# Kernel tuning notes

Hardware: AMD Instinct MI355X
Metric: run time of the kernel (lower is better)

The kernel has to match this reference:

```python
import jax, jax.numpy as jnp
import numpy as np

RATIO = 0.5
TEMP = 0.1


def setup_inputs() -> dict:
    key = jax.random.key(0)
    k1, k2, k3 = jax.random.split(key, 3)
    B, D = 4096, 4096
    im = jax.random.normal(k1, (B, D), dtype=jnp.float32)
    s = jax.random.normal(k2, (2 * B, D), dtype=jnp.float32)
    sims_local = jax.random.normal(k3, (B, 2 * B), dtype=jnp.float32)
    return {"im": im, "s": s, "sims_local": sims_local}


def reference(im, s, sims_local):
    B = im.shape[0]
    # fused global + local similarity: [B, 2B]
    sim = RATIO * sims_local + (1.0 - RATIO) * (im @ s.T)
    diag = jnp.diagonal(sim[:, :B])  # positives, [B]
    # vectorized replacement of the python double loop: zero out second-half
    # columns that exceed the row's diagonal (diagonal lives in first half,
    # so updates never feed back into the comparison -> exact equivalence).
    second = jnp.where(sim[:, B:] > diag[:, None], 0.0, sim[:, B:])
    sim = jnp.concatenate([sim[:, :B], second], axis=1)

    # i2t: logits per row = [positive (diag), all other 2B-1 entries];
    # CE with label 0 == logsumexp(full row) - positive (permutation-invariant).
    logits_i2t = sim / TEMP
    loss_i2t = jnp.mean(jax.nn.logsumexp(logits_i2t, axis=1) - diag / TEMP)

    # t2i: transpose, keep first B rows -> first block transposed, [B, B]
    t = sim[:, :B].T
    logits_t2i = t / TEMP
    loss_t2i = jnp.mean(jax.nn.logsumexp(logits_t2i, axis=1) - jnp.diagonal(t) / TEMP)

    return loss_i2t + loss_t2i
```

## Files before the change

### kernel.cpp

```cpp
#include <hip/hip_runtime.h>
#include <hip/hip_bf16.h>

typedef __attribute__((ext_vector_type(8))) short short8;
typedef __attribute__((ext_vector_type(4))) float floatx4;

#define B_ROWS 4096
#define N_COLS 8192
#define K_DIM  4096
#define INV_T  10.0f

__device__ __forceinline__ unsigned pack2bf16(float a, float b) {
    unsigned lo = (__float_as_uint(a) + 0x8000u) >> 16;
    unsigned hi = (__float_as_uint(b) + 0x8000u) & 0xFFFF0000u;
    return lo | hi;
}

__device__ __forceinline__ void gload_lds16(const void* g, void* l) {
    __builtin_amdgcn_global_load_lds(
        (const __attribute__((address_space(1))) void*)g,
        (__attribute__((address_space(3))) void*)l,
        16, 0, 0);
}

__global__ __launch_bounds__(256) void convert_diag_kernel(
    const float* __restrict__ im, const float* __restrict__ s,
    const float* __restrict__ sims,
    unsigned short* __restrict__ im_b, unsigned short* __restrict__ s_b,
    float* __restrict__ diag)
{
    const int row = blockIdx.x;
    const float4* srow = (const float4*)(s + (size_t)row * K_DIM);
    uint4* sb = (uint4*)(s_b + (size_t)row * K_DIM);
    const bool has_im = row < B_ROWS;
    const float4* arow = (const float4*)(im + (size_t)row * K_DIM);
    uint4* ab = (uint4*)(im_b + (size_t)row * K_DIM);

    float sum = 0.f;
    for (int i = threadIdx.x; i < K_DIM / 8; i += 256) {
        float4 y0 = srow[2 * i], y1 = srow[2 * i + 1];
        sb[i] = make_uint4(pack2bf16(y0.x, y0.y), pack2bf16(y0.z, y0.w),
                           pack2bf16(y1.x, y1.y), pack2bf16(y1.z, y1.w));
        if (has_im) {
            float4 x0 = arow[2 * i], x1 = arow[2 * i + 1];
            ab[i] = make_uint4(pack2bf16(x0.x, x0.y), pack2bf16(x0.z, x0.w),
                               pack2bf16(x1.x, x1.y), pack2bf16(x1.z, x1.w));
            sum += x0.x * y0.x + x0.y * y0.y + x0.z * y0.z + x0.w * y0.w;
            sum += x1.x * y1.x + x1.y * y1.y + x1.z * y1.z + x1.w * y1.w;
        }
    }
    if (has_im) {
        #pragma unroll
        for (int off = 1; off < 64; off <<= 1) sum += __shfl_xor(sum, off, 64);
        __shared__ float wsum[4];
        const int lane = threadIdx.x & 63, wid = threadIdx.x >> 6;
        if (lane == 0) wsum[wid] = sum;
        __syncthreads();
        if (threadIdx.x == 0) {
            float tot = wsum[0] + wsum[1] + wsum[2] + wsum[3];
            diag[row] = 0.5f * sims[(size_t)row * N_COLS + row] + 0.5f * tot;
        }
    }
}

__global__ __launch_bounds__(256, 3) void gemm_loss_bf16_kernel(
    const unsigned short* __restrict__ im_b, const unsigned short* __restrict__ s_b,
    const float* __restrict__ sims, const float* __restrict__ diag,
    float* __restrict__ pi2t_m, float* __restrict__ pi2t_l,
    float* __restrict__ pt2i_m, float* __restrict__ pt2i_l)
{
    const int jt = blockIdx.x;
    const int it = blockIdx.y;
    const int tid = threadIdx.x;
    const int wid = tid >> 6, lane = tid & 63;
    const int wr = wid >> 1, wc = wid & 1;
    const int q = lane >> 4, cl = lane & 15;

    __shared__ __align__(16) unsigned short Asm[2][128 * 32];
    __shared__ __align__(16) unsigned short Bsm[2][128 * 32];
    __shared__ float sm_m[2][128], sm_l[2][128];
    __shared__ float sc_m[2][128], sc_l[2][128];

    const int r0 = (wid * 2 + 0) * 16 + (lane >> 2);
    const int r1 = (wid * 2 + 1) * 16 + (lane >> 2);
    const int kg = (((lane & 3) ^ ((lane >> 3) & 3))) * 8;
    const unsigned short* gA0 = im_b + (size_t)(it * 128 + r0) * K_DIM + kg;
    const unsigned short* gA1 = im_b + (size_t)(it * 128 + r1) * K_DIM + kg;
    const unsigned short* gB0 = s_b + (size_t)(jt * 128 + r0) * K_DIM + kg;
    const unsigned short* gB1 = s_b + (size_t)(jt * 128 + r1) * K_DIM + kg;
    const int lo0 = (wid * 2 + 0) * 512;
    const int lo1 = (wid * 2 + 1) * 512;

    const int swA = (q ^ ((cl >> 1) & 3)) * 8;
    int roffA[4], roffB[4];
    #pragma unroll
    for (int t = 0; t < 4; ++t) {
        roffA[t] = (wr * 64 + t * 16 + cl) * 32 + swA;
        roffB[t] = (wc * 64 + t * 16 + cl) * 32 + swA;
    }

    floatx4 acc[4][4];
    #pragma unroll
    for (int i = 0; i < 4; ++i)
        #pragma unroll
        for (int j = 0; j < 4; ++j) acc[i][j] = (floatx4){0.f, 0.f, 0.f, 0.f};

    gload_lds16(gA0, &Asm[0][lo0]);
    gload_lds16(gA1, &Asm[0][lo1]);
    gload_lds16(gB0, &Bsm[0][lo0]);
    gload_lds16(gB1, &Bsm[0][lo1]);
    gA0 += 32; gA1 += 32; gB0 += 32; gB1 += 32;

    for (int kt = 0; kt < 128; ++kt) {
        const int cur = kt & 1;
        __syncthreads();
        if (kt < 127) {
            const int nxt = cur ^ 1;
            gload_lds16(gA0, &Asm[nxt][lo0]);
            gload_lds16(gA1, &Asm[nxt][lo1]);
            gload_lds16(gB0, &Bsm[nxt][lo0]);
            gload_lds16(gB1, &Bsm[nxt][lo1]);
            gA0 += 32; gA1 += 32; gB0 += 32; gB1 += 32;
        }
        short8 av[4], bv[4];
        #pragma unroll
        for (int ty = 0; ty < 4; ++ty)
            av[ty] = *(const short8*)&Asm[cur][roffA[ty]];
        #pragma unroll
        for (int tx = 0; tx < 4; ++tx)
            bv[tx] = *(const short8*)&Bsm[cur][roffB[tx]];
        #pragma unroll
        for (int ty = 0; ty < 4; ++ty)
            #pragma unroll
            for (int tx = 0; tx < 4; ++tx)
                acc[ty][tx] = __builtin_amdgcn_mfma_f32_16x16x32_bf16(av[ty], bv[tx], acc[ty][tx], 0, 0, 0);
    }

    const int row_base = it * 128 + wr * 64;
    const int col_base = jt * 128 + wc * 64;
    const bool second_half = (jt >= 32);

    float dv[4][4];
    #pragma unroll
    for (int ty = 0; ty < 4; ++ty)
        #pragma unroll
        for (int r = 0; r < 4; ++r)
            dv[ty][r] = diag[row_base + ty * 16 + q * 4 + r];

    #pragma unroll
    for (int ty = 0; ty < 4; ++ty) {
        #pragma unroll
        for (int tx = 0; tx < 4; ++tx) {
            const int col = col_base + tx * 16 + cl;
            #pragma unroll
            for (int r = 0; r < 4; ++r) {
                const int row = row_base + ty * 16 + q * 4 + r;
                float v = 0.5f * sims[(size_t)row * N_COLS + col] + 0.5f * acc[ty][tx][r];
                if (second_half && v > dv[ty][r]) v = 0.f;
                acc[ty][tx][r] = v * INV_T;
            }
        }
    }

    #pragma unroll
    for (int ty = 0; ty < 4; ++ty) {
        #pragma unroll
        for (int r = 0; r < 4; ++r) {
            float mx = fmaxf(fmaxf(acc[ty][0][r], acc[ty][1][r]),
                             fmaxf(acc[ty][2][r], acc[ty][3][r]));
            #pragma unroll
            for (int off = 1; off < 16; off <<= 1) mx = fmaxf(mx, __shfl_xor(mx, off, 64));
            float sum = 0.f;
            #pragma unroll
            for (int tx = 0; tx < 4; ++tx) sum += __expf(acc[ty][tx][r] - mx);
            #pragma unroll
            for (int off = 1; off < 16; off <<= 1) sum += __shfl_xor(sum, off, 64);
            if (cl == 0) {
                sm_m[wc][wr * 64 + ty * 16 + q * 4 + r] = mx;
                sm_l[wc][wr * 64 + ty * 16 + q * 4 + r] = sum;
            }
        }
    }

    if (!second_half) {
        #pragma unroll
        for (int tx = 0; tx < 4; ++tx) {
            float mx = -3.4e38f;
            #pragma unroll
            for (int ty = 0; ty < 4; ++ty)
                #pragma unroll
                for (int r = 0; r < 4; ++r) mx = fmaxf(mx, acc[ty][tx][r]);
            mx = fmaxf(mx, __shfl_xor(mx, 16, 64));
            mx = fmaxf(mx, __shfl_xor(mx, 32, 64));
            float sum = 0.f;
            #pragma unroll
            for (int ty = 0; ty < 4; ++ty)
                #pragma unroll
                for (int r = 0; r < 4; ++r) sum += __expf(acc[ty][tx][r] - mx);
            sum += __shfl_xor(sum, 16, 64);
            sum += __shfl_xor(sum, 32, 64);
            if (q == 0) {
                sc_m[wr][wc * 64 + tx * 16 + cl] = mx;
                sc_l[wr][wc * 64 + tx * 16 + cl] = sum;
            }
        }
    }

    __syncthreads();

    if (tid < 128) {
        float m0 = sm_m[0][tid], m1 = sm_m[1][tid];
        float mm = fmaxf(m0, m1);
        float ll = sm_l[0][tid] * __expf(m0 - mm) + sm_l[1][tid] * __expf(m1 - mm);
        pi2t_m[(size_t)jt * B_ROWS + it * 128 + tid] = mm;
        pi2t_l[(size_t)jt * B_ROWS + it * 128 + tid] = ll;
    } else if (!second_half) {
        const int t2 = tid - 128;
        float m0 = sc_m[0][t2], m1 = sc_m[1][t2];
        float mm = fmaxf(m0, m1);
        float ll = sc_l[0][t2] * __expf(m0 - mm) + sc_l[1][t2] * __expf(m1 - mm);
        pt2i_m[(size_t)it * B_ROWS + jt * 128 + t2] = mm;
        pt2i_l[(size_t)it * B_ROWS + jt * 128 + t2] = ll;
    }
}

__global__ __launch_bounds__(256) void diag_kernel(
    const float* __restrict__ im, const float* __restrict__ s,
    const float* __restrict__ sims, float* __restrict__ diag)
{
    const int row = blockIdx.x;
    const float4* a = (const float4*)(im + (size_t)row * K_DIM);
    const float4* b = (const float4*)(s  + (size_t)row * K_DIM);
    float sum = 0.f;
    for (int i = threadIdx.x; i < K_DIM / 4; i += 256) {
        float4 x = a[i], y = b[i];
        sum += x.x * y.x + x.y * y.y + x.z * y.z + x.w * y.w;
    }
    #pragma unroll
    for (int off = 1; off < 64; off <<= 1) sum += __shfl_xor(sum, off, 64);
    __shared__ float wsum[4];
    const int lane = threadIdx.x & 63, wid = threadIdx.x >> 6;
    if (lane == 0) wsum[wid] = sum;
    __syncthreads();
    if (threadIdx.x == 0) {
        float tot = wsum[0] + wsum[1] + wsum[2] + wsum[3];
        diag[row] = 0.5f * sims[(size_t)row * N_COLS + row] + 0.5f * tot;
    }
}

__global__ __launch_bounds__(256) void gemm_loss_kernel(
    const float* __restrict__ im, const float* __restrict__ s,
    const float* __restrict__ sims, const float* __restrict__ diag,
    float* __restrict__ pi2t_m, float* __restrict__ pi2t_l,
    float* __restrict__ pt2i_m, float* __restrict__ pt2i_l)
{
    const int jt = blockIdx.x;
    const int it = blockIdx.y;
    const int tid = threadIdx.x;
    const int wid = tid >> 6, lane = tid & 63;
    const int wr = wid >> 1, wc = wid & 1;
    const int q = lane >> 4, cl = lane & 15;

    __shared__ __align__(16) unsigned short Asm[128 * 32];
    __shared__ __align__(16) unsigned short Bsm[128 * 32];
    __shared__ float sm_m[2][128], sm_l[2][128];
    __shared__ float sc_m[2][128], sc_l[2][128];

    const int g0 = tid, g1 = tid + 256;
    const int r0 = g0 >> 2, c0 = (g0 & 3) * 8;
    const int r1 = g1 >> 2, c1 = (g1 & 3) * 8;
    const float* a0 = im + (size_t)(it * 128 + r0) * K_DIM + c0;
    const float* a1 = im + (size_t)(it * 128 + r1) * K_DIM + c1;
    const float* b0 = s  + (size_t)(jt * 128 + r0) * K_DIM + c0;
    const float* b1 = s  + (size_t)(jt * 128 + r1) * K_DIM + c1;
    const int la0 = r0 * 32 + c0, la1 = r1 * 32 + c1;

    floatx4 acc[4][4];
    #pragma unroll
    for (int i = 0; i < 4; ++i)
        #pragma unroll
        for (int j = 0; j < 4; ++j) acc[i][j] = (floatx4){0.f, 0.f, 0.f, 0.f};

    for (int kt = 0; kt < 128; ++kt) {
        float4 xa0 = *(const float4*)a0;
        float4 xa1 = *(const float4*)(a0 + 4);
        float4 ya0 = *(const float4*)a1;
        float4 ya1 = *(const float4*)(a1 + 4);
        float4 xb0 = *(const float4*)b0;
        float4 xb1 = *(const float4*)(b0 + 4);
        float4 yb0 = *(const float4*)b1;
        float4 yb1 = *(const float4*)(b1 + 4);
        a0 += 32; a1 += 32; b0 += 32; b1 += 32;
        __syncthreads();
        *(uint4*)&Asm[la0] = make_uint4(pack2bf16(xa0.x, xa0.y), pack2bf16(xa0.z, xa0.w),
                                        pack2bf16(xa1.x, xa1.y), pack2bf16(xa1.z, xa1.w));
        *(uint4*)&Asm[la1] = make_uint4(pack2bf16(ya0.x, ya0.y), pack2bf16(ya0.z, ya0.w),
                                        pack2bf16(ya1.x, ya1.y), pack2bf16(ya1.z, ya1.w));
        *(uint4*)&Bsm[la0] = make_uint4(pack2bf16(xb0.x, xb0.y), pack2bf16(xb0.z, xb0.w),
                                        pack2bf16(xb1.x, xb1.y), pack2bf16(xb1.z, xb1.w));
        *(uint4*)&Bsm[la1] = make_uint4(pack2bf16(yb0.x, yb0.y), pack2bf16(yb0.z, yb0.w),
                                        pack2bf16(yb1.x, yb1.y), pack2bf16(yb1.z, yb1.w));
        __syncthreads();
        short8 av[4], bv[4];
        #pragma unroll
        for (int ty = 0; ty < 4; ++ty)
            av[ty] = *(const short8*)&Asm[(wr * 64 + ty * 16 + cl) * 32 + q * 8];
        #pragma unroll
        for (int tx = 0; tx < 4; ++tx)
            bv[tx] = *(const short8*)&Bsm[(wc * 64 + tx * 16 + cl) * 32 + q * 8];
        #pragma unroll
        for (int ty = 0; ty < 4; ++ty)
            #pragma unroll
            for (int tx = 0; tx < 4; ++tx)
                acc[ty][tx] = __builtin_amdgcn_mfma_f32_16x16x32_bf16(av[ty], bv[tx], acc[ty][tx], 0, 0, 0);
    }

    const int row_base = it * 128 + wr * 64;
    const int col_base = jt * 128 + wc * 64;
    const bool second_half = (jt >= 32);

    float dv[4][4];
    #pragma unroll
    for (int ty = 0; ty < 4; ++ty)
        #pragma unroll
        for (int r = 0; r < 4; ++r)
            dv[ty][r] = diag[row_base + ty * 16 + q * 4 + r];

    #pragma unroll
    for (int ty = 0; ty < 4; ++ty) {
        #pragma unroll
        for (int tx = 0; tx < 4; ++tx) {
            const int col = col_base + tx * 16 + cl;
            #pragma unroll
            for (int r = 0; r < 4; ++r) {
                const int row = row_base + ty * 16 + q * 4 + r;
                float v = 0.5f * sims[(size_t)row * N_COLS + col] + 0.5f * acc[ty][tx][r];
                if (second_half && v > dv[ty][r]) v = 0.f;
                acc[ty][tx][r] = v * INV_T;
            }
        }
    }

    #pragma unroll
    for (int ty = 0; ty < 4; ++ty) {
        #pragma unroll
        for (int r = 0; r < 4; ++r) {
            float mx = fmaxf(fmaxf(acc[ty][0][r], acc[ty][1][r]),
                             fmaxf(acc[ty][2][r], acc[ty][3][r]));
            #pragma unroll
            for (int off = 1; off < 16; off <<= 1) mx = fmaxf(mx, __shfl_xor(mx, off, 64));
            float sum = 0.f;
            #pragma unroll
            for (int tx = 0; tx < 4; ++tx) sum += __expf(acc[ty][tx][r] - mx);
            #pragma unroll
            for (int off = 1; off < 16; off <<= 1) sum += __shfl_xor(sum, off, 64);
            if (cl == 0) {
                sm_m[wc][wr * 64 + ty * 16 + q * 4 + r] = mx;
                sm_l[wc][wr * 64 + ty * 16 + q * 4 + r] = sum;
            }
        }
    }

    if (!second_half) {
        #pragma unroll
        for (int tx = 0; tx < 4; ++tx) {
            float mx = -3.4e38f;
            #pragma unroll
            for (int ty = 0; ty < 4; ++ty)
                #pragma unroll
                for (int r = 0; r < 4; ++r) mx = fmaxf(mx, acc[ty][tx][r]);
            mx = fmaxf(mx, __shfl_xor(mx, 16, 64));
            mx = fmaxf(mx, __shfl_xor(mx, 32, 64));
            float sum = 0.f;
            #pragma unroll
            for (int ty = 0; ty < 4; ++ty)
                #pragma unroll
                for (int r = 0; r < 4; ++r) sum += __expf(acc[ty][tx][r] - mx);
            sum += __shfl_xor(sum, 16, 64);
            sum += __shfl_xor(sum, 32, 64);
            if (q == 0) {
                sc_m[wr][wc * 64 + tx * 16 + cl] = mx;
                sc_l[wr][wc * 64 + tx * 16 + cl] = sum;
            }
        }
    }

    __syncthreads();

    if (tid < 128) {
        float m0 = sm_m[0][tid], m1 = sm_m[1][tid];
        float mm = fmaxf(m0, m1);
        float ll = sm_l[0][tid] * __expf(m0 - mm) + sm_l[1][tid] * __expf(m1 - mm);
        pi2t_m[(size_t)jt * B_ROWS + it * 128 + tid] = mm;
        pi2t_l[(size_t)jt * B_ROWS + it * 128 + tid] = ll;
    } else if (!second_half) {
        const int t2 = tid - 128;
        float m0 = sc_m[0][t2], m1 = sc_m[1][t2];
        float mm = fmaxf(m0, m1);
        float ll = sc_l[0][t2] * __expf(m0 - mm) + sc_l[1][t2] * __expf(m1 - mm);
        pt2i_m[(size_t)it * B_ROWS + jt * 128 + t2] = mm;
        pt2i_l[(size_t)it * B_ROWS + jt * 128 + t2] = ll;
    }
}

__global__ __launch_bounds__(256) void combine_kernel(
    const float* __restrict__ pi2t_m, const float* __restrict__ pi2t_l,
    const float* __restrict__ pt2i_m, const float* __restrict__ pt2i_l,
    const float* __restrict__ diag, float* __restrict__ pblk)
{
    const int gid = blockIdx.x * 256 + threadIdx.x;
    float term;
    if (gid < B_ROWS) {
        const int row = gid;
        float m = pi2t_m[row], l = pi2t_l[row];
        for (int ct = 1; ct < 64; ++ct) {
            float m2 = pi2t_m[(size_t)ct * B_ROWS + row];
            float l2 = pi2t_l[(size_t)ct * B_ROWS + row];
            float nm = fmaxf(m, m2);
            l = l * __expf(m - nm) + l2 * __expf(m2 - nm);
            m = nm;
        }
        term = m + __logf(l) - diag[row] * INV_T;
    } else {
        const int col = gid - B_ROWS;
        float m = pt2i_m[col], l = pt2i_l[col];
        for (int rt = 1; rt < 32; ++rt) {
            float m2 = pt2i_m[(size_t)rt * B_ROWS + col];
            float l2 = pt2i_l[(size_t)rt * B_ROWS + col];
            float nm = fmaxf(m, m2);
            l = l * __expf(m - nm) + l2 * __expf(m2 - nm);
            m = nm;
        }
        term = m + __logf(l) - diag[col] * INV_T;
    }
    #pragma unroll
    for (int off = 1; off < 64; off <<= 1) term += __shfl_xor(term, off, 64);
    __shared__ float bsum[4];
    if ((threadIdx.x & 63) == 0) bsum[threadIdx.x >> 6] = term;
    __syncthreads();
    if (threadIdx.x == 0) pblk[blockIdx.x] = bsum[0] + bsum[1] + bsum[2] + bsum[3];
}

__global__ void finalize_kernel(const float* __restrict__ pblk, float* __restrict__ out) {
    float v = (threadIdx.x < 32) ? pblk[threadIdx.x] : 0.f;
    #pragma unroll
    for (int off = 1; off < 64; off <<= 1) v += __shfl_xor(v, off, 64);
    if (threadIdx.x == 0) out[0] = v * (1.0f / 4096.0f);
}

extern "C" void kernel_launch(void* const* d_in, const int* in_sizes, int n_in,
                              void* d_out, int out_size, void* d_ws, size_t ws_size,
                              hipStream_t stream)
{
    const float* im   = (const float*)d_in[0];
    const float* s    = (const float*)d_in[1];
    const float* sims = (const float*)d_in[2];
    float* out = (float*)d_out;

    const size_t im_b_bytes = (size_t)B_ROWS * K_DIM * 2;
    const size_t s_b_bytes  = (size_t)N_COLS * K_DIM * 2;
    const size_t f32_bytes  = (4096 + 2 * 64 * 4096 + 2 * 32 * 4096 + 32) * sizeof(float);
    const size_t need = im_b_bytes + s_b_bytes + f32_bytes;

    if (ws_size >= need) {
        unsigned short* im_b = (unsigned short*)d_ws;
        unsigned short* s_b  = (unsigned short*)((char*)d_ws + im_b_bytes);
        float* fbase  = (float*)((char*)d_ws + im_b_bytes + s_b_bytes);
        float* diag   = fbase;
        float* pi2t_m = diag + 4096;
        float* pi2t_l = pi2t_m + 64 * 4096;
        float* pt2i_m = pi2t_l + 64 * 4096;
        float* pt2i_l = pt2i_m + 32 * 4096;
        float* pblk   = pt2i_l + 32 * 4096;

        convert_diag_kernel<<<N_COLS, 256, 0, stream>>>(im, s, sims, im_b, s_b, diag);
        gemm_loss_bf16_kernel<<<dim3(64, 32), 256, 0, stream>>>(im_b, s_b, sims, diag,
                                                                pi2t_m, pi2t_l, pt2i_m, pt2i_l);
        combine_kernel<<<32, 256, 0, stream>>>(pi2t_m, pi2t_l, pt2i_m, pt2i_l, diag, pblk);
        finalize_kernel<<<1, 64, 0, stream>>>(pblk, out);
    } else {
        float* ws = (float*)d_ws;
        float* diag   = ws;
        float* pi2t_m = diag + 4096;
        float* pi2t_l = pi2t_m + 64 * 4096;
        float* pt2i_m = pi2t_l + 64 * 4096;
        float* pt2i_l = pt2i_m + 32 * 4096;
        float* pblk   = pt2i_l + 32 * 4096;

        diag_kernel<<<4096, 256, 0, stream>>>(im, s, sims, diag);
        gemm_loss_kernel<<<dim3(64, 32), 256, 0, stream>>>(im, s, sims, diag,
                                                           pi2t_m, pi2t_l, pt2i_m, pt2i_l);
        combine_kernel<<<32, 256, 0, stream>>>(pi2t_m, pi2t_l, pt2i_m, pt2i_l, diag, pblk);
        finalize_kernel<<<1, 64, 0, stream>>>(pblk, out);
    }
}
```

Baseline: 678.4 us.

## Swizzle GEMM tile order, raise occupancy, rebalance convert, fuse finalize via atomic

The GEMM grid becomes 1D, and tiles are remapped into 4x4 supertiles so that neighbouring workgroups share A/B panels in L2. Launch bounds go from 3 to 4 waves-per-EU hint. The convert kernel is split into im+diag blocks and blocks that each convert two extra s rows, with the loops fully unrolled. The finalize kernel is replaced by an atomicAdd into a memset output, which saves a launch but makes the float summation order nondeterministic.

```diff
diff --git a/kernel.cpp b/kernel.cpp
--- a/kernel.cpp
+++ b/kernel.cpp
@@ -28,27 +28,26 @@
     unsigned short* __restrict__ im_b, unsigned short* __restrict__ s_b,
     float* __restrict__ diag)
 {
-    const int row = blockIdx.x;
-    const float4* srow = (const float4*)(s + (size_t)row * K_DIM);
-    uint4* sb = (uint4*)(s_b + (size_t)row * K_DIM);
-    const bool has_im = row < B_ROWS;
-    const float4* arow = (const float4*)(im + (size_t)row * K_DIM);
-    uint4* ab = (uint4*)(im_b + (size_t)row * K_DIM);
-
-    float sum = 0.f;
-    for (int i = threadIdx.x; i < K_DIM / 8; i += 256) {
-        float4 y0 = srow[2 * i], y1 = srow[2 * i + 1];
-        sb[i] = make_uint4(pack2bf16(y0.x, y0.y), pack2bf16(y0.z, y0.w),
-                           pack2bf16(y1.x, y1.y), pack2bf16(y1.z, y1.w));
-        if (has_im) {
+    const int bid = blockIdx.x;
+    if (bid < B_ROWS) {
+        const int row = bid;
+        const float4* arow = (const float4*)(im + (size_t)row * K_DIM);
+        const float4* srow = (const float4*)(s  + (size_t)row * K_DIM);
+        uint4* ab = (uint4*)(im_b + (size_t)row * K_DIM);
+        uint4* sb = (uint4*)(s_b + (size_t)row * K_DIM);
+        float sum = 0.f;
+        #pragma unroll
+        for (int ii = 0; ii < 2; ++ii) {
+            const int i = threadIdx.x + ii * 256;
+            float4 y0 = srow[2 * i], y1 = srow[2 * i + 1];
             float4 x0 = arow[2 * i], x1 = arow[2 * i + 1];
+            sb[i] = make_uint4(pack2bf16(y0.x, y0.y), pack2bf16(y0.z, y0.w),
+                               pack2bf16(y1.x, y1.y), pack2bf16(y1.z, y1.w));
             ab[i] = make_uint4(pack2bf16(x0.x, x0.y), pack2bf16(x0.z, x0.w),
                                pack2bf16(x1.x, x1.y), pack2bf16(x1.z, x1.w));
             sum += x0.x * y0.x + x0.y * y0.y + x0.z * y0.z + x0.w * y0.w;
             sum += x1.x * y1.x + x1.y * y1.y + x1.z * y1.z + x1.w * y1.w;
         }
-    }
-    if (has_im) {
         #pragma unroll
         for (int off = 1; off < 64; off <<= 1) sum += __shfl_xor(sum, off, 64);
         __shared__ float wsum[4];
@@ -59,17 +58,35 @@
             float tot = wsum[0] + wsum[1] + wsum[2] + wsum[3];
             diag[row] = 0.5f * sims[(size_t)row * N_COLS + row] + 0.5f * tot;
         }
-    }
-}
-
-__global__ __launch_bounds__(256, 3) void gemm_loss_bf16_kernel(
+    } else {
+        const int r0 = B_ROWS + 2 * (bid - B_ROWS);
+        #pragma unroll
+        for (int rr = 0; rr < 2; ++rr) {
+            const int row = r0 + rr;
+            const float4* srow = (const float4*)(s + (size_t)row * K_DIM);
+            uint4* sb = (uint4*)(s_b + (size_t)row * K_DIM);
+            #pragma unroll
+            for (int ii = 0; ii < 2; ++ii) {
+                const int i = threadIdx.x + ii * 256;
+                float4 y0 = srow[2 * i], y1 = srow[2 * i + 1];
+                sb[i] = make_uint4(pack2bf16(y0.x, y0.y), pack2bf16(y0.z, y0.w),
+                                   pack2bf16(y1.x, y1.y), pack2bf16(y1.z, y1.w));
+            }
+        }
+    }
+}
+
+__global__ __launch_bounds__(256, 4) void gemm_loss_bf16_kernel(
     const unsigned short* __restrict__ im_b, const unsigned short* __restrict__ s_b,
     const float* __restrict__ sims, const float* __restrict__ diag,
     float* __restrict__ pi2t_m, float* __restrict__ pi2t_l,
     float* __restrict__ pt2i_m, float* __restrict__ pt2i_l)
 {
-    const int jt = blockIdx.x;
-    const int it = blockIdx.y;
+    const int bid = blockIdx.x;
+    const int sid = bid >> 4, sub = bid & 15;
+    const int it = (sid >> 4) * 4 + (sub >> 2);
+    const int jt = (sid & 15) * 4 + (sub & 3);
+
     const int tid = threadIdx.x;
     const int wid = tid >> 6, lane = tid & 63;
     const int wr = wid >> 1, wc = wid & 1;
@@ -405,7 +422,7 @@
 __global__ __launch_bounds__(256) void combine_kernel(
     const float* __restrict__ pi2t_m, const float* __restrict__ pi2t_l,
     const float* __restrict__ pt2i_m, const float* __restrict__ pt2i_l,
-    const float* __restrict__ diag, float* __restrict__ pblk)
+    const float* __restrict__ diag, float* __restrict__ out)
 {
     const int gid = blockIdx.x * 256 + threadIdx.x;
     float term;
@@ -437,14 +454,8 @@
     __shared__ float bsum[4];
     if ((threadIdx.x & 63) == 0) bsum[threadIdx.x >> 6] = term;
     __syncthreads();
-    if (threadIdx.x == 0) pblk[blockIdx.x] = bsum[0] + bsum[1] + bsum[2] + bsum[3];
-}
-
-__global__ void finalize_kernel(const float* __restrict__ pblk, float* __restrict__ out) {
-    float v = (threadIdx.x < 32) ? pblk[threadIdx.x] : 0.f;
-    #pragma unroll
-    for (int off = 1; off < 64; off <<= 1) v += __shfl_xor(v, off, 64);
-    if (threadIdx.x == 0) out[0] = v * (1.0f / 4096.0f);
+    if (threadIdx.x == 0)
+        atomicAdd(out, (bsum[0] + bsum[1] + bsum[2] + bsum[3]) * (1.0f / 4096.0f));
 }
 
 extern "C" void kernel_launch(void* const* d_in, const int* in_sizes, int n_in,
@@ -458,8 +469,10 @@
 
     const size_t im_b_bytes = (size_t)B_ROWS * K_DIM * 2;
     const size_t s_b_bytes  = (size_t)N_COLS * K_DIM * 2;
-    const size_t f32_bytes  = (4096 + 2 * 64 * 4096 + 2 * 32 * 4096 + 32) * sizeof(float);
+    const size_t f32_bytes  = (4096 + 2 * 64 * 4096 + 2 * 32 * 4096) * sizeof(float);
     const size_t need = im_b_bytes + s_b_bytes + f32_bytes;
+
+    hipMemsetAsync(out, 0, sizeof(float), stream);
 
     if (ws_size >= need) {
         unsigned short* im_b = (unsigned short*)d_ws;
@@ -470,13 +483,11 @@
         float* pi2t_l = pi2t_m + 64 * 4096;
         float* pt2i_m = pi2t_l + 64 * 4096;
         float* pt2i_l = pt2i_m + 32 * 4096;
-        float* pblk   = pt2i_l + 32 * 4096;
-
-        convert_diag_kernel<<<N_COLS, 256, 0, stream>>>(im, s, sims, im_b, s_b, diag);
-        gemm_loss_bf16_kernel<<<dim3(64, 32), 256, 0, stream>>>(im_b, s_b, sims, diag,
-                                                                pi2t_m, pi2t_l, pt2i_m, pt2i_l);
-        combine_kernel<<<32, 256, 0, stream>>>(pi2t_m, pi2t_l, pt2i_m, pt2i_l, diag, pblk);
-        finalize_kernel<<<1, 64, 0, stream>>>(pblk, out);
+
+        convert_diag_kernel<<<6144, 256, 0, stream>>>(im, s, sims, im_b, s_b, diag);
+        gemm_loss_bf16_kernel<<<2048, 256, 0, stream>>>(im_b, s_b, sims, diag,
+                                                        pi2t_m, pi2t_l, pt2i_m, pt2i_l);
+        combine_kernel<<<32, 256, 0, stream>>>(pi2t_m, pi2t_l, pt2i_m, pt2i_l, diag, out);
     } else {
         float* ws = (float*)d_ws;
         float* diag   = ws;
@@ -484,12 +495,10 @@
         float* pi2t_l = pi2t_m + 64 * 4096;
         float* pt2i_m = pi2t_l + 64 * 4096;
         float* pt2i_l = pt2i_m + 32 * 4096;
-        float* pblk   = pt2i_l + 32 * 4096;
 
         diag_kernel<<<4096, 256, 0, stream>>>(im, s, sims, diag);
         gemm_loss_kernel<<<dim3(64, 32), 256, 0, stream>>>(im, s, sims, diag,
                                                            pi2t_m, pi2t_l, pt2i_m, pt2i_l);
-        combine_kernel<<<32, 256, 0, stream>>>(pi2t_m, pi2t_l, pt2i_m, pt2i_l, diag, pblk);
-        finalize_kernel<<<1, 64, 0, stream>>>(pblk, out);
-    }
-}
+        combine_kernel<<<32, 256, 0, stream>>>(pi2t_m, pi2t_l, pt2i_m, pt2i_l, diag, out);
+    }
+}
```

Result: slower. 818.7 us (+20.7%).
